# Kernel tuning notes

Hardware: AMD Instinct MI355X
Metric: run time of the kernel (lower is better)

## Reference

```python
import jax, jax.numpy as jnp
import numpy as np

MAX_PATH_DISTANCE = 5


def setup_inputs() -> dict:
    key = jax.random.key(0)
    k1, k2, k3, k4, k5 = jax.random.split(key, 5)
    N = 8192
    E = 4_000_000
    x = jax.random.normal(k1, (N, 128), dtype=jnp.float32)
    src = jax.random.randint(k2, (E,), 0, N, dtype=jnp.int64)
    dst = jax.random.randint(k3, (E,), 0, N, dtype=jnp.int64)
    # path lengths; original computes len(paths[src][dst]) >= 1
    path_len = jax.random.randint(k4, (E,), 0, 6, dtype=jnp.int64)
    # learned parameter b of shape [max_path_distance]
    b = jax.random.normal(k5, (MAX_PATH_DISTANCE,), dtype=jnp.float32)
    return {"x": x, "b": b, "src": src, "dst": dst, "path_len": path_len}


def reference(x, b, src, dst, path_len):
    N = x.shape[0]
    # index = min(len, max_path_distance) - 1, clamped to valid range
    idx = jnp.clip(path_len, 1, MAX_PATH_DISTANCE) - 1  # [E]
    vals = b[idx]  # [E] gather from tiny table
    spatial = jnp.zeros((N, N), dtype=b.dtype)
    spatial = spatial.at[src, dst].set(vals)  # scatter into pairwise bias matrix
    return spatial
```

## Files before the change

### kernel.cpp

```cpp
#include <hip/hip_runtime.h>

#define MAX_PATH_DISTANCE 5
#define NROW 8192
#define ROWS_PER_BKT 128
#define NBKT 64
#define SLICES 17
#define EPB 4096
#define CAPB (SLICES * EPB)
#define CAPR 768
#define BLK 512
#define NWAVE 8
#define EPT 8


__device__ __forceinline__ int clamp_bidx(int pl) {
    int c = pl < 1 ? 1 : (pl > MAX_PATH_DISTANCE ? MAX_PATH_DISTANCE : pl);
    return c - 1;
}

__global__ __launch_bounds__(BLK) void se_coarse(
        const int4* __restrict__ src4, const int4* __restrict__ dst4,
        const int4* __restrict__ plen4,
        unsigned long long* __restrict__ bkt,
        unsigned int* __restrict__ bkt_cur, int E4) {
    __shared__ __align__(16) unsigned long long stage[EPB];
    __shared__ unsigned int hist[NWAVE][NBKT], wb[NWAVE][NBKT];
    __shared__ unsigned int base_l[NBKT], gbase[NBKT], s_total;
    const int tid = threadIdx.x;
    const int w   = tid >> 6;
    const int q0  = blockIdx.x * (EPB / 4);

    for (int i = tid; i < NWAVE * NBKT; i += BLK) (&hist[0][0])[i] = 0u;
    __syncthreads();

    unsigned long long ent[EPT];
#pragma unroll
    for (int g = 0; g < 2; ++g) {
        int q = q0 + g * BLK + tid;
        if (q < E4) {
            int4 s = src4[q], d = dst4[q], p = plen4[q];
            int ss[4] = {s.x, s.y, s.z, s.w};
            int dd[4] = {d.x, d.y, d.z, d.w};
            int pp[4] = {p.x, p.y, p.z, p.w};
#pragma unroll
            for (int c = 0; c < 4; ++c) {
                int e = (q << 2) + c;
                unsigned int key = ((unsigned int)(e + 1) << 3)
                                 | (unsigned int)clamp_bidx(pp[c]);
                unsigned long long v =
                      ((unsigned long long)(unsigned int)ss[c] << 38)
                    | ((unsigned long long)(unsigned int)dd[c] << 25)
                    | (unsigned long long)key;
                ent[g * 4 + c] = v;
                atomicAdd(&hist[w][(unsigned int)(v >> 45)], 1u);
            }
        } else {
#pragma unroll
            for (int c = 0; c < 4; ++c) ent[g * 4 + c] = 0ull;
        }
    }
    __syncthreads();

    if (tid < NBKT) {
        unsigned int t = 0;
#pragma unroll
        for (int ww = 0; ww < NWAVE; ++ww) t += hist[ww][tid];
        base_l[tid] = t;
    }
    __syncthreads();
    if (tid == 0) {
        unsigned int run = 0;
        for (int i = 0; i < NBKT; ++i) {
            unsigned int t = base_l[i]; base_l[i] = run; run += t;
        }
        s_total = run;
    }
    __syncthreads();
    if (tid < NBKT) {
        unsigned int t = base_l[tid], tot = 0;
#pragma unroll
        for (int ww = 0; ww < NWAVE; ++ww) {
            wb[ww][tid] = t; t += hist[ww][tid]; tot += hist[ww][tid];
        }
        gbase[tid] = atomicAdd(&bkt_cur[tid], tot);
    }
    __syncthreads();

#pragma unroll
    for (int j = 0; j < EPT; ++j) {
        if (ent[j]) {
            unsigned int bb = (unsigned int)(ent[j] >> 45);
            unsigned int p  = atomicAdd(&wb[w][bb], 1u);
            stage[p] = ent[j];
        }
    }
    __syncthreads();

    const unsigned int total = s_total;
    for (unsigned int i = tid; i < total; i += BLK) {
        unsigned long long v = stage[i];
        unsigned int bb  = (unsigned int)(v >> 45);
        unsigned int pos = gbase[bb] + (i - base_l[bb]);
        if (pos < CAPB) bkt[(size_t)bb * CAPB + pos] = v;
    }
}

__global__ __launch_bounds__(BLK) void se_fine(
        const unsigned long long* __restrict__ bkt,
        const unsigned int* __restrict__ bkt_cur,
        unsigned long long* __restrict__ rbins,
        unsigned int* __restrict__ rcur) {
    __shared__ __align__(16) unsigned long long stage[EPB];
    __shared__ unsigned int hist[NWAVE][ROWS_PER_BKT];
    __shared__ unsigned int wb[NWAVE][ROWS_PER_BKT];
    __shared__ unsigned int base_l[ROWS_PER_BKT], gbase[ROWS_PER_BKT], s_total;
    const int tid = threadIdx.x;
    const int w   = tid >> 6;
    const int b   = blockIdx.x / SLICES;
    const int sl  = blockIdx.x % SLICES;

    unsigned int cnt = bkt_cur[b]; if (cnt > CAPB) cnt = CAPB;
    const int i0 = sl * EPB;
    int n = (int)cnt - i0;
    if (n <= 0) return;
    if (n > EPB) n = EPB;

    for (int i = tid; i < NWAVE * ROWS_PER_BKT; i += BLK) (&hist[0][0])[i] = 0u;
    __syncthreads();

    const unsigned long long* bp = bkt + (size_t)b * CAPB + i0;
    unsigned long long ent[EPT];
#pragma unroll
    for (int j = 0; j < EPT; ++j) {
        int i = j * BLK + tid;
        ent[j] = 0ull;
        if (i < n) {
            ent[j] = bp[i];
            atomicAdd(&hist[w][(unsigned int)(ent[j] >> 38) & 127u], 1u);
        }
    }
    __syncthreads();

    if (tid < ROWS_PER_BKT) {
        unsigned int t = 0;
#pragma unroll
        for (int ww = 0; ww < NWAVE; ++ww) t += hist[ww][tid];
        base_l[tid] = t;
    }
    __syncthreads();
    if (tid == 0) {
        unsigned int run = 0;
        for (int i = 0; i < ROWS_PER_BKT; ++i) {
            unsigned int t = base_l[i]; base_l[i] = run; run += t;
        }
        s_total = run;
    }
    __syncthreads();
    if (tid < ROWS_PER_BKT) {
        unsigned int t = base_l[tid], tot = 0;
#pragma unroll
        for (int ww = 0; ww < NWAVE; ++ww) {
            wb[ww][tid] = t; t += hist[ww][tid]; tot += hist[ww][tid];
        }
        gbase[tid] = atomicAdd(&rcur[b * ROWS_PER_BKT + tid], tot);
    }
    __syncthreads();

#pragma unroll
    for (int j = 0; j < EPT; ++j) {
        if (ent[j]) {
            unsigned int rl = (unsigned int)(ent[j] >> 38) & 127u;
            unsigned int p  = atomicAdd(&wb[w][rl], 1u);
            stage[p] = ent[j];
        }
    }
    __syncthreads();

    const unsigned int total = s_total;
    for (unsigned int i = tid; i < total; i += BLK) {
        unsigned long long v = stage[i];
        unsigned int s   = (unsigned int)((v >> 38) & 0x1FFFu);
        unsigned int rl  = s & 127u;
        unsigned int pos = gbase[rl] + (i - base_l[rl]);
        if (pos < CAPR) rbins[(size_t)s * CAPR + pos] = v;
    }
}

__global__ __launch_bounds__(BLK) void se_rows(
        const unsigned long long* __restrict__ rbins,
        const unsigned int* __restrict__ rcur,
        const float* __restrict__ b,
        float* __restrict__ out) {
    __shared__ unsigned int lds[NROW];
    const int r = blockIdx.x, tid = threadIdx.x;

    for (int i = tid; i < NROW; i += BLK) lds[i] = 0u;

    unsigned int cnt = rcur[r]; if (cnt > CAPR) cnt = CAPR;
    const unsigned long long* bp = rbins + (size_t)r * CAPR;

    unsigned long long e0 = 0ull, e1 = 0ull;
    if ((unsigned int)tid < cnt)        e0 = bp[tid];
    if ((unsigned int)tid + BLK < cnt)  e1 = bp[tid + BLK];
    __syncthreads();

    if (e0) atomicMax(&lds[(unsigned int)((e0 >> 25) & 0x1FFFu)],
                      (unsigned int)(e0 & 0x1FFFFFFu));
    if (e1) atomicMax(&lds[(unsigned int)((e1 >> 25) & 0x1FFFu)],
                      (unsigned int)(e1 & 0x1FFFFFFu));
    __syncthreads();

    if (e0) {
        unsigned int key = (unsigned int)(e0 & 0x1FFFFFFu);
        unsigned int d   = (unsigned int)((e0 >> 25) & 0x1FFFu);
        if (lds[d] == key) lds[d] = __float_as_uint(b[key & 7u]);
    }
    if (e1) {
        unsigned int key = (unsigned int)(e1 & 0x1FFFFFFu);
        unsigned int d   = (unsigned int)((e1 >> 25) & 0x1FFFu);
        if (lds[d] == key) lds[d] = __float_as_uint(b[key & 7u]);
    }
    __syncthreads();

    float4* out4 = reinterpret_cast<float4*>(out + (size_t)r * NROW);
    const float4* l4 = reinterpret_cast<const float4*>(lds);
#pragma unroll
    for (int k = 0; k < NROW / 4 / BLK; ++k) out4[k * BLK + tid] = l4[k * BLK + tid];
}


__global__ void se_scatter_keys(const int* __restrict__ src,
                                const int* __restrict__ dst,
                                const int* __restrict__ plen,
                                unsigned int* __restrict__ out,
                                int E, int N) {
    int e = blockIdx.x * blockDim.x + threadIdx.x;
    if (e >= E) return;
    unsigned int key = ((unsigned int)(e + 1) << 3)
                     | (unsigned int)clamp_bidx(plen[e]);
    atomicMax(&out[(size_t)src[e] * (size_t)N + (size_t)dst[e]], key);
}

__global__ void se_resolve(const int* __restrict__ src,
                           const int* __restrict__ dst,
                           const int* __restrict__ plen,
                           const float* __restrict__ b,
                           unsigned int* __restrict__ out,
                           int E, int N) {
    int e = blockIdx.x * blockDim.x + threadIdx.x;
    if (e >= E) return;
    unsigned int key = ((unsigned int)(e + 1) << 3)
                     | (unsigned int)clamp_bidx(plen[e]);
    size_t off = (size_t)src[e] * (size_t)N + (size_t)dst[e];
    if (out[off] == key) {
        reinterpret_cast<float*>(out)[off] = b[key & 7u];
    }
}


extern "C" void kernel_launch(void* const* d_in, const int* in_sizes, int n_in,
                              void* d_out, int out_size, void* d_ws, size_t ws_size,
                              hipStream_t stream) {
    const float* b    = (const float*)d_in[1];
    const int*   src  = (const int*)d_in[2];
    const int*   dst  = (const int*)d_in[3];
    const int*   plen = (const int*)d_in[4];

    const int N = in_sizes[0] / 128;
    const int E = in_sizes[2];

    const size_t rbins_bytes = (size_t)NROW * CAPR * sizeof(unsigned long long);
    const size_t bkt_bytes   = (size_t)NBKT * CAPB * sizeof(unsigned long long);
    const size_t cur_bytes   = (size_t)(NROW + NBKT) * sizeof(unsigned int);
    const size_t need = rbins_bytes + bkt_bytes + cur_bytes;

    if (N == NROW && (unsigned int)E < (1u << 22) && (E % 4) == 0 &&
        ws_size >= need) {
        unsigned long long* rbins = (unsigned long long*)d_ws;
        unsigned long long* bktp  = (unsigned long long*)((char*)d_ws + rbins_bytes);
        unsigned int* rcur = (unsigned int*)((char*)d_ws + rbins_bytes + bkt_bytes);
        unsigned int* bcur = rcur + NROW;

        hipMemsetAsync(rcur, 0, cur_bytes, stream);
        se_coarse<<<(E + EPB - 1) / EPB, BLK, 0, stream>>>(
            (const int4*)src, (const int4*)dst, (const int4*)plen,
            bktp, bcur, E / 4);
        se_fine<<<NBKT * SLICES, BLK, 0, stream>>>(bktp, bcur, rbins, rcur);
        se_rows<<<NROW, BLK, 0, stream>>>(rbins, rcur, b, (float*)d_out);
    } else {
        const int block = 256;
        const int gridE = (E + block - 1) / block;
        hipMemsetAsync(d_out, 0, (size_t)out_size * sizeof(float), stream);
        se_scatter_keys<<<gridE, block, 0, stream>>>(src, dst, plen,
                                                     (unsigned int*)d_out, E, N);
        se_resolve<<<gridE, block, 0, stream>>>(src, dst, plen, b,
                                                (unsigned int*)d_out, E, N);
    }
}
```

Baseline: 112.0 us.

## Process two rows per block in se_rows and halve fine-pass histogram copies

se_rows now handles two output rows per block, issuing the global loads for both rows' entries up front so the second row's load latency hides behind the first row's LDS work and store. The grid is halved. In se_fine, the per-wave histograms are merged into four groups of 128 threads, which shrinks LDS footprint and the number of prefix/scan iterations but adds more atomic contention per histogram. The two-row version adds extra barriers and serialises the two rows within a block.

Result: faster. 107.9 us (-3.6%).

```diff
diff --git a/kernel.cpp b/kernel.cpp
--- a/kernel.cpp
+++ b/kernel.cpp
@@ -10,6 +10,7 @@
 #define CAPR 768
 #define BLK 512
 #define NWAVE 8
+#define NHG 4
 #define EPT 8
 
 
@@ -111,11 +112,11 @@
         unsigned long long* __restrict__ rbins,
         unsigned int* __restrict__ rcur) {
     __shared__ __align__(16) unsigned long long stage[EPB];
-    __shared__ unsigned int hist[NWAVE][ROWS_PER_BKT];
-    __shared__ unsigned int wb[NWAVE][ROWS_PER_BKT];
+    __shared__ unsigned int hist[NHG][ROWS_PER_BKT];
+    __shared__ unsigned int wb[NHG][ROWS_PER_BKT];
     __shared__ unsigned int base_l[ROWS_PER_BKT], gbase[ROWS_PER_BKT], s_total;
     const int tid = threadIdx.x;
-    const int w   = tid >> 6;
+    const int w   = tid >> 7;
     const int b   = blockIdx.x / SLICES;
     const int sl  = blockIdx.x % SLICES;
 
@@ -125,7 +126,7 @@
     if (n <= 0) return;
     if (n > EPB) n = EPB;
 
-    for (int i = tid; i < NWAVE * ROWS_PER_BKT; i += BLK) (&hist[0][0])[i] = 0u;
+    for (int i = tid; i < NHG * ROWS_PER_BKT; i += BLK) (&hist[0][0])[i] = 0u;
     __syncthreads();
 
     const unsigned long long* bp = bkt + (size_t)b * CAPB + i0;
@@ -144,7 +145,7 @@
     if (tid < ROWS_PER_BKT) {
         unsigned int t = 0;
 #pragma unroll
-        for (int ww = 0; ww < NWAVE; ++ww) t += hist[ww][tid];
+        for (int ww = 0; ww < NHG; ++ww) t += hist[ww][tid];
         base_l[tid] = t;
     }
     __syncthreads();
@@ -159,7 +160,7 @@
     if (tid < ROWS_PER_BKT) {
         unsigned int t = base_l[tid], tot = 0;
 #pragma unroll
-        for (int ww = 0; ww < NWAVE; ++ww) {
+        for (int ww = 0; ww < NHG; ++ww) {
             wb[ww][tid] = t; t += hist[ww][tid]; tot += hist[ww][tid];
         }
         gbase[tid] = atomicAdd(&rcur[b * ROWS_PER_BKT + tid], tot);
@@ -189,43 +190,75 @@
 __global__ __launch_bounds__(BLK) void se_rows(
         const unsigned long long* __restrict__ rbins,
         const unsigned int* __restrict__ rcur,
-        const float* __restrict__ b,
+        const float* __restrict__ bias,
         float* __restrict__ out) {
     __shared__ unsigned int lds[NROW];
-    const int r = blockIdx.x, tid = threadIdx.x;
+    const int tid = threadIdx.x;
+    const int r0  = blockIdx.x * 2;
+
+    unsigned int cntA = rcur[r0];     if (cntA > CAPR) cntA = CAPR;
+    unsigned int cntB = rcur[r0 + 1]; if (cntB > CAPR) cntB = CAPR;
+    const unsigned long long* bpA = rbins + (size_t)r0 * CAPR;
+    const unsigned long long* bpB = bpA + CAPR;
+
+    unsigned long long a0 = 0ull, a1 = 0ull, b0 = 0ull, b1 = 0ull;
+    if ((unsigned int)tid < cntA)        a0 = bpA[tid];
+    if ((unsigned int)tid + BLK < cntA)  a1 = bpA[tid + BLK];
+    if ((unsigned int)tid < cntB)        b0 = bpB[tid];
+    if ((unsigned int)tid + BLK < cntB)  b1 = bpB[tid + BLK];
 
     for (int i = tid; i < NROW; i += BLK) lds[i] = 0u;
-
-    unsigned int cnt = rcur[r]; if (cnt > CAPR) cnt = CAPR;
-    const unsigned long long* bp = rbins + (size_t)r * CAPR;
-
-    unsigned long long e0 = 0ull, e1 = 0ull;
-    if ((unsigned int)tid < cnt)        e0 = bp[tid];
-    if ((unsigned int)tid + BLK < cnt)  e1 = bp[tid + BLK];
-    __syncthreads();
-
-    if (e0) atomicMax(&lds[(unsigned int)((e0 >> 25) & 0x1FFFu)],
-                      (unsigned int)(e0 & 0x1FFFFFFu));
-    if (e1) atomicMax(&lds[(unsigned int)((e1 >> 25) & 0x1FFFu)],
-                      (unsigned int)(e1 & 0x1FFFFFFu));
-    __syncthreads();
-
-    if (e0) {
-        unsigned int key = (unsigned int)(e0 & 0x1FFFFFFu);
-        unsigned int d   = (unsigned int)((e0 >> 25) & 0x1FFFu);
-        if (lds[d] == key) lds[d] = __float_as_uint(b[key & 7u]);
-    }
-    if (e1) {
-        unsigned int key = (unsigned int)(e1 & 0x1FFFFFFu);
-        unsigned int d   = (unsigned int)((e1 >> 25) & 0x1FFFu);
-        if (lds[d] == key) lds[d] = __float_as_uint(b[key & 7u]);
-    }
-    __syncthreads();
-
-    float4* out4 = reinterpret_cast<float4*>(out + (size_t)r * NROW);
-    const float4* l4 = reinterpret_cast<const float4*>(lds);
-#pragma unroll
-    for (int k = 0; k < NROW / 4 / BLK; ++k) out4[k * BLK + tid] = l4[k * BLK + tid];
+    __syncthreads();
+    if (a0) atomicMax(&lds[(unsigned int)((a0 >> 25) & 0x1FFFu)],
+                      (unsigned int)(a0 & 0x1FFFFFFu));
+    if (a1) atomicMax(&lds[(unsigned int)((a1 >> 25) & 0x1FFFu)],
+                      (unsigned int)(a1 & 0x1FFFFFFu));
+    __syncthreads();
+    if (a0) {
+        unsigned int key = (unsigned int)(a0 & 0x1FFFFFFu);
+        unsigned int d   = (unsigned int)((a0 >> 25) & 0x1FFFu);
+        if (lds[d] == key) lds[d] = __float_as_uint(bias[key & 7u]);
+    }
+    if (a1) {
+        unsigned int key = (unsigned int)(a1 & 0x1FFFFFFu);
+        unsigned int d   = (unsigned int)((a1 >> 25) & 0x1FFFu);
+        if (lds[d] == key) lds[d] = __float_as_uint(bias[key & 7u]);
+    }
+    __syncthreads();
+    {
+        float4* out4 = reinterpret_cast<float4*>(out + (size_t)r0 * NROW);
+        const float4* l4 = reinterpret_cast<const float4*>(lds);
+#pragma unroll
+        for (int k = 0; k < NROW / 4 / BLK; ++k)
+            out4[k * BLK + tid] = l4[k * BLK + tid];
+    }
+    __syncthreads();
+
+    for (int i = tid; i < NROW; i += BLK) lds[i] = 0u;
+    __syncthreads();
+    if (b0) atomicMax(&lds[(unsigned int)((b0 >> 25) & 0x1FFFu)],
+                      (unsigned int)(b0 & 0x1FFFFFFu));
+    if (b1) atomicMax(&lds[(unsigned int)((b1 >> 25) & 0x1FFFu)],
+                      (unsigned int)(b1 & 0x1FFFFFFu));
+    __syncthreads();
+    if (b0) {
+        unsigned int key = (unsigned int)(b0 & 0x1FFFFFFu);
+        unsigned int d   = (unsigned int)((b0 >> 25) & 0x1FFFu);
+        if (lds[d] == key) lds[d] = __float_as_uint(bias[key & 7u]);
+    }
+    if (b1) {
+        unsigned int key = (unsigned int)(b1 & 0x1FFFFFFu);
+        unsigned int d   = (unsigned int)((b1 >> 25) & 0x1FFFu);
+        if (lds[d] == key) lds[d] = __float_as_uint(bias[key & 7u]);
+    }
+    __syncthreads();
+    {
+        float4* out4 = reinterpret_cast<float4*>(out + (size_t)(r0 + 1) * NROW);
+        const float4* l4 = reinterpret_cast<const float4*>(lds);
+#pragma unroll
+        for (int k = 0; k < NROW / 4 / BLK; ++k)
+            out4[k * BLK + tid] = l4[k * BLK + tid];
+    }
 }
 
 
@@ -286,7 +319,7 @@
             (const int4*)src, (const int4*)dst, (const int4*)plen,
             bktp, bcur, E / 4);
         se_fine<<<NBKT * SLICES, BLK, 0, stream>>>(bktp, bcur, rbins, rcur);
-        se_rows<<<NROW, BLK, 0, stream>>>(rbins, rcur, b, (float*)d_out);
+        se_rows<<<NROW / 2, BLK, 0, stream>>>(rbins, rcur, b, (float*)d_out);
     } else {
         const int block = 256;
         const int gridE = (E + block - 1) / block;
```

## Process four rows per block, resolve bias at write-out, nontemporal stores

Applied to the files above, without the earlier changes.

se_rows now handles four rows per block, preloading all their bin entries up front and reusing one LDS row buffer. The separate resolve pass, which re-read LDS and gathered bias from global memory per winning entry, is replaced by a lookup into a shared bias table during the vectorized write-out. Output rows are written with nontemporal stores to avoid polluting cache on the 256 MB write. se_fine also halves its per-wave histogram count to 4 groups of 128 threads, which shrinks LDS and the prefix loops but raises atomic contention.

Result: faster. 105.7 us (-5.6%).

```diff
diff --git a/kernel.cpp b/kernel.cpp
--- a/kernel.cpp
+++ b/kernel.cpp
@@ -10,7 +10,11 @@
 #define CAPR 768
 #define BLK 512
 #define NWAVE 8
+#define NHG 4
 #define EPT 8
+#define RPB 4
+
+typedef float f32x4 __attribute__((ext_vector_type(4)));
 
 
 __device__ __forceinline__ int clamp_bidx(int pl) {
@@ -111,11 +115,11 @@
         unsigned long long* __restrict__ rbins,
         unsigned int* __restrict__ rcur) {
     __shared__ __align__(16) unsigned long long stage[EPB];
-    __shared__ unsigned int hist[NWAVE][ROWS_PER_BKT];
-    __shared__ unsigned int wb[NWAVE][ROWS_PER_BKT];
+    __shared__ unsigned int hist[NHG][ROWS_PER_BKT];
+    __shared__ unsigned int wb[NHG][ROWS_PER_BKT];
     __shared__ unsigned int base_l[ROWS_PER_BKT], gbase[ROWS_PER_BKT], s_total;
     const int tid = threadIdx.x;
-    const int w   = tid >> 6;
+    const int w   = tid >> 7;
     const int b   = blockIdx.x / SLICES;
     const int sl  = blockIdx.x % SLICES;
 
@@ -125,7 +129,7 @@
     if (n <= 0) return;
     if (n > EPB) n = EPB;
 
-    for (int i = tid; i < NWAVE * ROWS_PER_BKT; i += BLK) (&hist[0][0])[i] = 0u;
+    for (int i = tid; i < NHG * ROWS_PER_BKT; i += BLK) (&hist[0][0])[i] = 0u;
     __syncthreads();
 
     const unsigned long long* bp = bkt + (size_t)b * CAPB + i0;
@@ -144,7 +148,7 @@
     if (tid < ROWS_PER_BKT) {
         unsigned int t = 0;
 #pragma unroll
-        for (int ww = 0; ww < NWAVE; ++ww) t += hist[ww][tid];
+        for (int ww = 0; ww < NHG; ++ww) t += hist[ww][tid];
         base_l[tid] = t;
     }
     __syncthreads();
@@ -159,7 +163,7 @@
     if (tid < ROWS_PER_BKT) {
         unsigned int t = base_l[tid], tot = 0;
 #pragma unroll
-        for (int ww = 0; ww < NWAVE; ++ww) {
+        for (int ww = 0; ww < NHG; ++ww) {
             wb[ww][tid] = t; t += hist[ww][tid]; tot += hist[ww][tid];
         }
         gbase[tid] = atomicAdd(&rcur[b * ROWS_PER_BKT + tid], tot);
@@ -188,44 +192,55 @@
 
 __global__ __launch_bounds__(BLK) void se_rows(
         const unsigned long long* __restrict__ rbins,
-        const unsigned int* __restrict__ rcur,
-        const float* __restrict__ b,
+        const uint4* __restrict__ rcur4,
+        const float* __restrict__ bias,
         float* __restrict__ out) {
     __shared__ unsigned int lds[NROW];
-    const int r = blockIdx.x, tid = threadIdx.x;
-
-    for (int i = tid; i < NROW; i += BLK) lds[i] = 0u;
-
-    unsigned int cnt = rcur[r]; if (cnt > CAPR) cnt = CAPR;
-    const unsigned long long* bp = rbins + (size_t)r * CAPR;
-
-    unsigned long long e0 = 0ull, e1 = 0ull;
-    if ((unsigned int)tid < cnt)        e0 = bp[tid];
-    if ((unsigned int)tid + BLK < cnt)  e1 = bp[tid + BLK];
-    __syncthreads();
-
-    if (e0) atomicMax(&lds[(unsigned int)((e0 >> 25) & 0x1FFFu)],
-                      (unsigned int)(e0 & 0x1FFFFFFu));
-    if (e1) atomicMax(&lds[(unsigned int)((e1 >> 25) & 0x1FFFu)],
-                      (unsigned int)(e1 & 0x1FFFFFFu));
-    __syncthreads();
-
-    if (e0) {
-        unsigned int key = (unsigned int)(e0 & 0x1FFFFFFu);
-        unsigned int d   = (unsigned int)((e0 >> 25) & 0x1FFFu);
-        if (lds[d] == key) lds[d] = __float_as_uint(b[key & 7u]);
-    }
-    if (e1) {
-        unsigned int key = (unsigned int)(e1 & 0x1FFFFFFu);
-        unsigned int d   = (unsigned int)((e1 >> 25) & 0x1FFFu);
-        if (lds[d] == key) lds[d] = __float_as_uint(b[key & 7u]);
-    }
-    __syncthreads();
-
-    float4* out4 = reinterpret_cast<float4*>(out + (size_t)r * NROW);
-    const float4* l4 = reinterpret_cast<const float4*>(lds);
-#pragma unroll
-    for (int k = 0; k < NROW / 4 / BLK; ++k) out4[k * BLK + tid] = l4[k * BLK + tid];
+    __shared__ float lbias[8];
+    const int tid = threadIdx.x;
+    const int r0  = blockIdx.x * RPB;
+
+    if (tid < 8) lbias[tid] = (tid < MAX_PATH_DISTANCE) ? bias[tid] : 0.0f;
+
+    uint4 cv = rcur4[blockIdx.x];
+    unsigned int cnt[RPB] = {cv.x, cv.y, cv.z, cv.w};
+#pragma unroll
+    for (int k = 0; k < RPB; ++k) if (cnt[k] > CAPR) cnt[k] = CAPR;
+
+    unsigned long long e0[RPB], e1[RPB];
+#pragma unroll
+    for (int k = 0; k < RPB; ++k) {
+        const unsigned long long* bp = rbins + (size_t)(r0 + k) * CAPR;
+        e0[k] = ((unsigned int)tid < cnt[k])       ? bp[tid]       : 0ull;
+        e1[k] = ((unsigned int)tid + BLK < cnt[k]) ? bp[tid + BLK] : 0ull;
+    }
+
+#pragma unroll
+    for (int k = 0; k < RPB; ++k) {
+        if (k) __syncthreads();
+        for (int i = tid; i < NROW; i += BLK) lds[i] = 0u;
+        __syncthreads();
+
+        if (e0[k]) atomicMax(&lds[(unsigned int)((e0[k] >> 25) & 0x1FFFu)],
+                             (unsigned int)(e0[k] & 0x1FFFFFFu));
+        if (e1[k]) atomicMax(&lds[(unsigned int)((e1[k] >> 25) & 0x1FFFu)],
+                             (unsigned int)(e1[k] & 0x1FFFFFFu));
+        __syncthreads();
+
+        float* orow = out + (size_t)(r0 + k) * NROW;
+        const uint4* l4 = reinterpret_cast<const uint4*>(lds);
+#pragma unroll
+        for (int q = 0; q < NROW / 4 / BLK; ++q) {
+            uint4 u = l4[q * BLK + tid];
+            f32x4 f;
+            f.x = u.x ? lbias[u.x & 7u] : 0.0f;
+            f.y = u.y ? lbias[u.y & 7u] : 0.0f;
+            f.z = u.z ? lbias[u.z & 7u] : 0.0f;
+            f.w = u.w ? lbias[u.w & 7u] : 0.0f;
+            __builtin_nontemporal_store(
+                f, reinterpret_cast<f32x4*>(orow) + q * BLK + tid);
+        }
+    }
 }
 
 
@@ -286,7 +301,8 @@
             (const int4*)src, (const int4*)dst, (const int4*)plen,
             bktp, bcur, E / 4);
         se_fine<<<NBKT * SLICES, BLK, 0, stream>>>(bktp, bcur, rbins, rcur);
-        se_rows<<<NROW, BLK, 0, stream>>>(rbins, rcur, b, (float*)d_out);
+        se_rows<<<NROW / RPB, BLK, 0, stream>>>(rbins, (const uint4*)rcur, b,
+                                                (float*)d_out);
     } else {
         const int block = 256;
         const int gridE = (E + block - 1) / block;
```
